# Performance work log

Hardware: AMD Instinct MI355X
Metric: run time of the kernel (lower is better)

Reference implementation:

```python
import jax, jax.numpy as jnp
import numpy as np

IN_DIM = 2
HID = 256
OUT_DIM = 1
B = 131072


def setup_inputs() -> dict:
    key = jax.random.key(0)
    ks = jax.random.split(key, 9)
    def glorot(k, shape):
        fan_in = shape[0]
        return jax.random.normal(k, shape, dtype=jnp.float32) / jnp.sqrt(jnp.float32(fan_in))
    return {
        "x": jax.random.normal(ks[0], (B, IN_DIM), dtype=jnp.float32),
        "W1": glorot(ks[1], (IN_DIM, HID)), "b1": jnp.zeros((HID,), jnp.float32),
        "W2": glorot(ks[2], (HID, HID)),    "b2": jnp.zeros((HID,), jnp.float32),
        "W3": glorot(ks[3], (HID, HID)),    "b3": jnp.zeros((HID,), jnp.float32),
        "W4": glorot(ks[4], (HID, OUT_DIM)),"b4": jnp.zeros((OUT_DIM,), jnp.float32),
    }


def reference(x, W1, b1, W2, b2, W3, b3, W4, b4):
    # Inner PINN model: tanh MLP, per-sample fn (IN_DIM,) -> (OUT_DIM,)
    def f(xi):
        h = jnp.tanh(xi @ W1 + b1)
        h = jnp.tanh(h @ W2 + b2)
        h = jnp.tanh(h @ W3 + b3)
        return h @ W4 + b4

    # Original layer computes full batch_jacobian then slices column 0.
    # Mathematically this is the directional derivative along e0, computed
    # here directly with forward-mode JVPs (same values, no wasted columns).
    e0 = jnp.zeros((IN_DIM,), x.dtype).at[0].set(1.0)

    def du_dx0(xi):  # (OUT_DIM,) : d u / d x[0]
        return jax.jvp(f, (xi,), (e0,))[1]

    def per_point(xi):
        u = f(xi)                                   # (OUT_DIM,)
        du, d2u = jax.jvp(du_dx0, (xi,), (e0,))     # du/dx0, d2u/dx0^2
        return u, du, d2u

    return jax.vmap(per_point)(x)  # each (B, OUT_DIM)
```

## Files before the change

kernel.cpp:

```cpp
#include <hip/hip_runtime.h>


#define HID 256
#define TM  32
#define LDK 264

typedef _Float16 half8 __attribute__((ext_vector_type(8)));
typedef _Float16 half4 __attribute__((ext_vector_type(4)));
typedef float    f32x4 __attribute__((ext_vector_type(4)));

__device__ __forceinline__ float fast_tanh(float z) {
    const float e = __expf(2.0f * z);
#if __has_builtin(__builtin_amdgcn_rcpf)
    const float r = __builtin_amdgcn_rcpf(e + 1.0f);
#else
    const float r = 1.0f / (e + 1.0f);
#endif
    return fmaf(-2.0f, r, 1.0f);
}

__global__ __launch_bounds__(256) void prep_w(const float* __restrict__ W2,
                                              const float* __restrict__ W3,
                                              _Float16* __restrict__ wsf) {
    const int t = blockIdx.x * 256 + threadIdx.x;
    const float* __restrict__ W = (t >> 13) ? W3 : W2;
    _Float16* hi = wsf + (size_t)(t >> 13) * 65536;
    const int r    = t & 8191;
    const int nt   = r >> 9;
    const int kc   = (r >> 6) & 7;
    const int lane = r & 63;
    const int row  = kc * 32 + ((lane >> 4) << 3);
    const int col  = nt * 16 + (lane & 15);
    half8 vh;
    #pragma unroll
    for (int j = 0; j < 8; ++j)
        vh[j] = (_Float16)W[(size_t)(row + j) * HID + col];
    *(half8*)&hi[(size_t)r * 8] = vh;
}

__global__ __launch_bounds__(512, 4) void pinn_mfma(
    const float* __restrict__ x,
    const float* __restrict__ W1, const float* __restrict__ b1,
    const float* __restrict__ b2, const float* __restrict__ b3,
    const float* __restrict__ W4, const float* __restrict__ b4,
    const _Float16* __restrict__ wsf,
    float* __restrict__ out, int B)
{
    __shared__ __align__(16) _Float16 Ahi[3][TM][LDK];
    __shared__ float psumW[8][3][TM];

    const int tid  = threadIdx.x;
    const int s0   = blockIdx.x * TM;
    const int lane = tid & 63;
    const int wave = tid >> 6;

    {
        const int m  = tid >> 4;
        const int k0 = (tid & 15) * 16;
        const float x0 = x[(s0 + m) * 2 + 0];
        const float x1 = x[(s0 + m) * 2 + 1];
        half8 vh[3][2];
        #pragma unroll
        for (int hfi = 0; hfi < 2; ++hfi) {
            #pragma unroll
            for (int j = 0; j < 8; ++j) {
                const int n = k0 + hfi * 8 + j;
                const float w0 = W1[n];
                const float w1 = W1[HID + n];
                const float z  = fmaf(x0, w0, fmaf(x1, w1, b1[n]));
                const float a  = fast_tanh(z);
                const float sN = 1.0f - a * a;
                const float ad  = sN * w0;
                const float add = -2.0f * a * ad * w0;
                vh[0][hfi][j] = (_Float16)a;
                vh[1][hfi][j] = (_Float16)ad;
                vh[2][hfi][j] = (_Float16)add;
            }
        }
        #pragma unroll
        for (int s = 0; s < 3; ++s) {
            *(half8*)&Ahi[s][m][k0]     = vh[s][0];
            *(half8*)&Ahi[s][m][k0 + 8] = vh[s][1];
        }
    }
    __syncthreads();

    const int ml = lane & 15;
    const int kq = (lane >> 4) * 8;
    const int u4 = (lane >> 4) * 4;

    #pragma unroll 1
    for (int layer = 0; layer < 2; ++layer) {
        const _Float16* __restrict__ Wh = wsf + (size_t)layer * 65536;

        f32x4 acc[3][2][2];
        #pragma unroll
        for (int s = 0; s < 3; ++s)
            #pragma unroll
            for (int nt = 0; nt < 2; ++nt)
                #pragma unroll
                for (int mt = 0; mt < 2; ++mt)
                    acc[s][nt][mt] = (f32x4){0.f, 0.f, 0.f, 0.f};

        #pragma unroll 1
        for (int kc = 0; kc < 8; ++kc) {
            half8 ah[3][2];
            #pragma unroll
            for (int s = 0; s < 3; ++s)
                #pragma unroll
                for (int mt = 0; mt < 2; ++mt)
                    ah[s][mt] = *(const half8*)&Ahi[s][mt * 16 + ml][kc * 32 + kq];
            #pragma unroll
            for (int nt = 0; nt < 2; ++nt) {
                const int strip = wave * 2 + nt;
                const size_t fi = ((size_t)((strip * 8 + kc) * 64 + lane)) * 8;
                const half8 wh = *(const half8*)&Wh[fi];
                #pragma unroll
                for (int mt = 0; mt < 2; ++mt) {
                    acc[0][nt][mt] = __builtin_amdgcn_mfma_f32_16x16x32_f16(wh, ah[0][mt], acc[0][nt][mt], 0, 0, 0);
                    acc[1][nt][mt] = __builtin_amdgcn_mfma_f32_16x16x32_f16(wh, ah[1][mt], acc[1][nt][mt], 0, 0, 0);
                    acc[2][nt][mt] = __builtin_amdgcn_mfma_f32_16x16x32_f16(wh, ah[2][mt], acc[2][nt][mt], 0, 0, 0);
                }
            }
        }

        __syncthreads();

        if (layer == 0) {
            #pragma unroll
            for (int nt = 0; nt < 2; ++nt) {
                const int ub = wave * 32 + nt * 16 + u4;
                const f32x4 bb = *(const f32x4*)&b2[ub];
                #pragma unroll
                for (int mt = 0; mt < 2; ++mt) {
                    half4 hv[3];
                    #pragma unroll
                    for (int r = 0; r < 4; ++r) {
                        const float z   = acc[0][nt][mt][r] + bb[r];
                        const float a   = fast_tanh(z);
                        const float sN  = 1.0f - a * a;
                        const float zd  = acc[1][nt][mt][r];
                        const float zdd = acc[2][nt][mt][r];
                        const float ad  = sN * zd;
                        const float add = fmaf(sN, zdd, -2.0f * a * ad * zd);
                        hv[0][r] = (_Float16)a;
                        hv[1][r] = (_Float16)ad;
                        hv[2][r] = (_Float16)add;
                    }
                    #pragma unroll
                    for (int s = 0; s < 3; ++s)
                        *(half4*)&Ahi[s][mt * 16 + ml][ub] = hv[s];
                }
            }
            __syncthreads();
        } else {
            float pd[3][2] = {{0.f, 0.f}, {0.f, 0.f}, {0.f, 0.f}};
            #pragma unroll
            for (int nt = 0; nt < 2; ++nt) {
                const int ub = wave * 32 + nt * 16 + u4;
                const f32x4 bb = *(const f32x4*)&b3[ub];
                const f32x4 w4 = *(const f32x4*)&W4[ub];
                #pragma unroll
                for (int mt = 0; mt < 2; ++mt) {
                    #pragma unroll
                    for (int r = 0; r < 4; ++r) {
                        const float z   = acc[0][nt][mt][r] + bb[r];
                        const float a   = fast_tanh(z);
                        const float sN  = 1.0f - a * a;
                        const float zd  = acc[1][nt][mt][r];
                        const float zdd = acc[2][nt][mt][r];
                        const float ad  = sN * zd;
                        const float add = fmaf(sN, zdd, -2.0f * a * ad * zd);
                        pd[0][mt] = fmaf(a,   w4[r], pd[0][mt]);
                        pd[1][mt] = fmaf(ad,  w4[r], pd[1][mt]);
                        pd[2][mt] = fmaf(add, w4[r], pd[2][mt]);
                    }
                }
            }
            #pragma unroll
            for (int s = 0; s < 3; ++s)
                #pragma unroll
                for (int mt = 0; mt < 2; ++mt) {
                    pd[s][mt] += __shfl_xor(pd[s][mt], 16, 64);
                    pd[s][mt] += __shfl_xor(pd[s][mt], 32, 64);
                }
            if (lane < 16) {
                #pragma unroll
                for (int s = 0; s < 3; ++s) {
                    psumW[wave][s][lane]      = pd[s][0];
                    psumW[wave][s][16 + lane] = pd[s][1];
                }
            }
        }
    }
    __syncthreads();

    if (tid < 96) {
        const int s = tid >> 5;
        const int m = tid & 31;
        float v = 0.f;
        #pragma unroll
        for (int w = 0; w < 8; ++w) v += psumW[w][s][m];
        if (s == 0) v += b4[0];
        out[(size_t)s * B + s0 + m] = v;
    }
}

extern "C" void kernel_launch(void* const* d_in, const int* in_sizes, int n_in,
                              void* d_out, int out_size, void* d_ws, size_t ws_size,
                              hipStream_t stream) {
    const float* x  = (const float*)d_in[0];
    const float* W1 = (const float*)d_in[1];
    const float* b1 = (const float*)d_in[2];
    const float* W2 = (const float*)d_in[3];
    const float* b2 = (const float*)d_in[4];
    const float* W3 = (const float*)d_in[5];
    const float* b3 = (const float*)d_in[6];
    const float* W4 = (const float*)d_in[7];
    const float* b4 = (const float*)d_in[8];
    float* out = (float*)d_out;

    const int B = in_sizes[0] / 2;

    prep_w<<<64, 256, 0, stream>>>(W2, W3, (_Float16*)d_ws);
    pinn_mfma<<<B / TM, 512, 0, stream>>>(x, W1, b1, b2, b3, W4, b4,
                                          (const _Float16*)d_ws, out, B);
}
```

Measured before the change: 187.3 us.

## Halve waves per block, widen per-wave N tiles, prefetch weights, swizzle LDS

Blocks drop from 8 waves to 4, and each wave now covers 64 output columns (4 N-tiles) instead of 32. Each LDS A-fragment load therefore feeds twice as many MFMAs. The weight fragments are re-laid out kc-major and software-prefetched one k-chunk ahead in registers, and the padded LDS rows are replaced by an XOR swizzle to avoid bank conflicts. The cost is many more accumulator registers (24 f32x4) and fewer waves per block, which may lower occupancy.

Result: faster. 174.8 us (-6.7%).

```diff
diff --git a/kernel.cpp b/kernel.cpp
--- a/kernel.cpp
+++ b/kernel.cpp
@@ -3,11 +3,12 @@
 
 #define HID 256
 #define TM  32
-#define LDK 264
 
 typedef _Float16 half8 __attribute__((ext_vector_type(8)));
 typedef _Float16 half4 __attribute__((ext_vector_type(4)));
 typedef float    f32x4 __attribute__((ext_vector_type(4)));
+
+#define MFMA16 __builtin_amdgcn_mfma_f32_16x16x32_f16
 
 __device__ __forceinline__ float fast_tanh(float z) {
     const float e = __expf(2.0f * z);
@@ -24,21 +25,21 @@
                                               _Float16* __restrict__ wsf) {
     const int t = blockIdx.x * 256 + threadIdx.x;
     const float* __restrict__ W = (t >> 13) ? W3 : W2;
-    _Float16* hi = wsf + (size_t)(t >> 13) * 65536;
-    const int r    = t & 8191;
-    const int nt   = r >> 9;
-    const int kc   = (r >> 6) & 7;
-    const int lane = r & 63;
-    const int row  = kc * 32 + ((lane >> 4) << 3);
-    const int col  = nt * 16 + (lane & 15);
+    _Float16* dst = wsf + (size_t)(t >> 13) * 65536;
+    const int r     = t & 8191;
+    const int kc    = r >> 10;
+    const int strip = (r >> 6) & 15;
+    const int lane  = r & 63;
+    const int row   = kc * 32 + ((lane >> 4) << 3);
+    const int col   = strip * 16 + (lane & 15);
     half8 vh;
     #pragma unroll
     for (int j = 0; j < 8; ++j)
         vh[j] = (_Float16)W[(size_t)(row + j) * HID + col];
-    *(half8*)&hi[(size_t)r * 8] = vh;
-}
-
-__global__ __launch_bounds__(512, 4) void pinn_mfma(
+    *(half8*)&dst[(size_t)r * 8] = vh;
+}
+
+__global__ __launch_bounds__(256, 2) void pinn_mfma(
     const float* __restrict__ x,
     const float* __restrict__ W1, const float* __restrict__ b1,
     const float* __restrict__ b2, const float* __restrict__ b3,
@@ -46,8 +47,8 @@
     const _Float16* __restrict__ wsf,
     float* __restrict__ out, int B)
 {
-    __shared__ __align__(16) _Float16 Ahi[3][TM][LDK];
-    __shared__ float psumW[8][3][TM];
+    __shared__ __align__(16) _Float16 Ahi[3 * 32 * 256];
+    __shared__ float psumW[4][3][TM];
 
     const int tid  = threadIdx.x;
     const int s0   = blockIdx.x * TM;
@@ -55,82 +56,104 @@
     const int wave = tid >> 6;
 
     {
-        const int m  = tid >> 4;
-        const int k0 = (tid & 15) * 16;
-        const float x0 = x[(s0 + m) * 2 + 0];
-        const float x1 = x[(s0 + m) * 2 + 1];
-        half8 vh[3][2];
-        #pragma unroll
-        for (int hfi = 0; hfi < 2; ++hfi) {
-            #pragma unroll
-            for (int j = 0; j < 8; ++j) {
-                const int n = k0 + hfi * 8 + j;
-                const float w0 = W1[n];
-                const float w1 = W1[HID + n];
-                const float z  = fmaf(x0, w0, fmaf(x1, w1, b1[n]));
-                const float a  = fast_tanh(z);
-                const float sN = 1.0f - a * a;
-                const float ad  = sN * w0;
-                const float add = -2.0f * a * ad * w0;
-                vh[0][hfi][j] = (_Float16)a;
-                vh[1][hfi][j] = (_Float16)ad;
-                vh[2][hfi][j] = (_Float16)add;
+        const int m  = (tid & 7) | (((tid >> 3) & 3) << 3);
+        const int k0 = (tid >> 5) << 5;
+        const float2 xv = *(const float2*)&x[(size_t)(s0 + m) * 2];
+        const float x0 = xv.x, x1 = xv.y;
+        half8 vh[3][4];
+        #pragma unroll
+        for (int q = 0; q < 4; ++q) {
+            #pragma unroll
+            for (int h = 0; h < 2; ++h) {
+                const int n = k0 + q * 8 + h * 4;
+                const f32x4 w0 = *(const f32x4*)&W1[n];
+                const f32x4 w1 = *(const f32x4*)&W1[HID + n];
+                const f32x4 bb = *(const f32x4*)&b1[n];
+                #pragma unroll
+                for (int r = 0; r < 4; ++r) {
+                    const float z  = fmaf(x0, w0[r], fmaf(x1, w1[r], bb[r]));
+                    const float a  = fast_tanh(z);
+                    const float sN = 1.0f - a * a;
+                    const float ad  = sN * w0[r];
+                    const float add = -2.0f * a * ad * w0[r];
+                    vh[0][q][h * 4 + r] = (_Float16)a;
+                    vh[1][q][h * 4 + r] = (_Float16)ad;
+                    vh[2][q][h * 4 + r] = (_Float16)add;
+                }
             }
         }
-        #pragma unroll
-        for (int s = 0; s < 3; ++s) {
-            *(half8*)&Ahi[s][m][k0]     = vh[s][0];
-            *(half8*)&Ahi[s][m][k0 + 8] = vh[s][1];
-        }
+        const int rkm = m & 7;
+        const int g0  = k0 >> 3;
+        #pragma unroll
+        for (int s = 0; s < 3; ++s)
+            #pragma unroll
+            for (int q = 0; q < 4; ++q)
+                *(half8*)&Ahi[s * 8192 + m * 256 + (((g0 + q) ^ rkm) << 3)] = vh[s][q];
     }
     __syncthreads();
 
     const int ml = lane & 15;
-    const int kq = (lane >> 4) * 8;
-    const int u4 = (lane >> 4) * 4;
+    const int hi = lane >> 4;
+    const int rk = ml & 7;
+    const int u4 = hi << 2;
+    const _Float16* __restrict__ Arow = &Ahi[ml * 256];
 
     #pragma unroll 1
     for (int layer = 0; layer < 2; ++layer) {
-        const _Float16* __restrict__ Wh = wsf + (size_t)layer * 65536;
-
-        f32x4 acc[3][2][2];
+        const _Float16* __restrict__ Wl =
+            wsf + ((size_t)layer << 16) + (wave << 11) + (lane << 3);
+
+        f32x4 acc[3][4][2];
         #pragma unroll
         for (int s = 0; s < 3; ++s)
             #pragma unroll
-            for (int nt = 0; nt < 2; ++nt)
+            for (int nt = 0; nt < 4; ++nt)
                 #pragma unroll
                 for (int mt = 0; mt < 2; ++mt)
                     acc[s][nt][mt] = (f32x4){0.f, 0.f, 0.f, 0.f};
 
+        half8 wcur[4];
+        #pragma unroll
+        for (int nt = 0; nt < 4; ++nt)
+            wcur[nt] = *(const half8*)&Wl[nt << 9];
+
         #pragma unroll 1
         for (int kc = 0; kc < 8; ++kc) {
-            half8 ah[3][2];
+            const int kn = (kc < 7) ? kc + 1 : 7;
+            const _Float16* __restrict__ Wk = Wl + (kn << 13);
+            half8 wnxt[4];
+            #pragma unroll
+            for (int nt = 0; nt < 4; ++nt)
+                wnxt[nt] = *(const half8*)&Wk[nt << 9];
+
+            const _Float16* __restrict__ Ap =
+                Arow + ((((kc << 2) | hi) ^ rk) << 3);
+            half8 af[3][2];
             #pragma unroll
             for (int s = 0; s < 3; ++s)
                 #pragma unroll
                 for (int mt = 0; mt < 2; ++mt)
-                    ah[s][mt] = *(const half8*)&Ahi[s][mt * 16 + ml][kc * 32 + kq];
-            #pragma unroll
-            for (int nt = 0; nt < 2; ++nt) {
-                const int strip = wave * 2 + nt;
-                const size_t fi = ((size_t)((strip * 8 + kc) * 64 + lane)) * 8;
-                const half8 wh = *(const half8*)&Wh[fi];
-                #pragma unroll
-                for (int mt = 0; mt < 2; ++mt) {
-                    acc[0][nt][mt] = __builtin_amdgcn_mfma_f32_16x16x32_f16(wh, ah[0][mt], acc[0][nt][mt], 0, 0, 0);
-                    acc[1][nt][mt] = __builtin_amdgcn_mfma_f32_16x16x32_f16(wh, ah[1][mt], acc[1][nt][mt], 0, 0, 0);
-                    acc[2][nt][mt] = __builtin_amdgcn_mfma_f32_16x16x32_f16(wh, ah[2][mt], acc[2][nt][mt], 0, 0, 0);
-                }
-            }
+                    af[s][mt] = *(const half8*)&Ap[s * 8192 + mt * 4096];
+
+            #pragma unroll
+            for (int nt = 0; nt < 4; ++nt)
+                #pragma unroll
+                for (int mt = 0; mt < 2; ++mt) {
+                    acc[0][nt][mt] = MFMA16(wcur[nt], af[0][mt], acc[0][nt][mt], 0, 0, 0);
+                    acc[1][nt][mt] = MFMA16(wcur[nt], af[1][mt], acc[1][nt][mt], 0, 0, 0);
+                    acc[2][nt][mt] = MFMA16(wcur[nt], af[2][mt], acc[2][nt][mt], 0, 0, 0);
+                }
+            #pragma unroll
+            for (int nt = 0; nt < 4; ++nt) wcur[nt] = wnxt[nt];
         }
 
-        __syncthreads();
-
         if (layer == 0) {
-            #pragma unroll
-            for (int nt = 0; nt < 2; ++nt) {
-                const int ub = wave * 32 + nt * 16 + u4;
+            __syncthreads();
+            #pragma unroll
+            for (int nt = 0; nt < 4; ++nt) {
+                const int ub  = (wave << 6) + (nt << 4) + u4;
                 const f32x4 bb = *(const f32x4*)&b2[ub];
+                const int gsw = (((ub >> 3) ^ rk) << 3) + (u4 & 4);
                 #pragma unroll
                 for (int mt = 0; mt < 2; ++mt) {
                     half4 hv[3];
@@ -147,17 +170,18 @@
                         hv[1][r] = (_Float16)ad;
                         hv[2][r] = (_Float16)add;
                     }
-                    #pragma unroll
-                    for (int s = 0; s < 3; ++s)
-                        *(half4*)&Ahi[s][mt * 16 + ml][ub] = hv[s];
+                    const int base = (mt * 16 + ml) * 256 + gsw;
+                    *(half4*)&Ahi[base]         = hv[0];
+                    *(half4*)&Ahi[8192  + base] = hv[1];
+                    *(half4*)&Ahi[16384 + base] = hv[2];
                 }
             }
             __syncthreads();
         } else {
             float pd[3][2] = {{0.f, 0.f}, {0.f, 0.f}, {0.f, 0.f}};
             #pragma unroll
-            for (int nt = 0; nt < 2; ++nt) {
-                const int ub = wave * 32 + nt * 16 + u4;
+            for (int nt = 0; nt < 4; ++nt) {
+                const int ub = (wave << 6) + (nt << 4) + u4;
                 const f32x4 bb = *(const f32x4*)&b3[ub];
                 const f32x4 w4 = *(const f32x4*)&W4[ub];
                 #pragma unroll
@@ -198,10 +222,9 @@
     if (tid < 96) {
         const int s = tid >> 5;
         const int m = tid & 31;
-        float v = 0.f;
-        #pragma unroll
-        for (int w = 0; w < 8; ++w) v += psumW[w][s][m];
-        if (s == 0) v += b4[0];
+        const float v = psumW[0][s][m] + psumW[1][s][m]
+                      + psumW[2][s][m] + psumW[3][s][m]
+                      + ((s == 0) ? b4[0] : 0.0f);
         out[(size_t)s * B + s0 + m] = v;
     }
 }
@@ -223,6 +246,6 @@
     const int B = in_sizes[0] / 2;
 
     prep_w<<<64, 256, 0, stream>>>(W2, W3, (_Float16*)d_ws);
-    pinn_mfma<<<B / TM, 512, 0, stream>>>(x, W1, b1, b2, b3, W4, b4,
+    pinn_mfma<<<B / TM, 256, 0, stream>>>(x, W1, b1, b2, b3, W4, b4,
                                           (const _Float16*)d_ws, out, B);
 }
```
